# Kernel optimization log

Hardware: AMD Instinct MI355X
Metric: run time of the kernel (lower is better)

The kernel has to match this reference:

```python
import jax, jax.numpy as jnp
import numpy as np

B, D_MODEL, FEAT = 2, 96, 128
SSM_RATIO, D_STATE, NDIR, CGROUP = 2.0, 16, 4, 12
D_INNER = int(SSM_RATIO * D_MODEL)  # 192


def _conv1x1(x, w):
    # x: (B, Cin, H, W), w: (Cout, Cin)
    return jnp.einsum('bchw,oc->bohw', x, w)


def _normalize_w(Gl, Gm, Gr):
    gl, gm, gr = jax.nn.sigmoid(Gl), jax.nn.sigmoid(Gm), jax.nn.sigmoid(Gr)
    s = gl + gm + gr
    # top row has no (i-1) neighbor, bottom row has no (i+1) neighbor
    s = s.at[:, :, 0, :].set(gm[:, :, 0, :] + gr[:, :, 0, :])
    s = s.at[:, :, -1, :].set(gl[:, :, -1, :] + gm[:, :, -1, :])
    s = jnp.maximum(s, 1e-7)
    return gl / s, gm / s, gr / s


def _spn_scan(X, l, Gl, Gm, Gr):
    # Gated tridiagonal 2D recurrence, left-to-right over W:
    # h[i,t] = l[i,t]*x[i,t] + Gl[i,t]*h[i-1,t-1] + Gm[i,t]*h[i,t-1] + Gr[i,t]*h[i+1,t-1]
    seq = tuple(jnp.moveaxis(a, -1, 0) for a in (X, l, Gl, Gm, Gr))  # (W, B, C, H)
    h0 = jnp.zeros(X.shape[:-1], X.dtype)  # (B, C, H)

    def step(h, t):
        x_t, l_t, gl_t, gm_t, gr_t = t
        zero = jnp.zeros_like(h[..., :1])
        h_up = jnp.concatenate([zero, h[..., :-1]], axis=-1)  # h[i-1]
        h_dn = jnp.concatenate([h[..., 1:], zero], axis=-1)   # h[i+1]
        h = l_t * x_t + gl_t * h_up + gm_t * h + gr_t * h_dn
        return h, h

    _, ys = jax.lax.scan(step, h0, seq)
    return jnp.moveaxis(ys, 0, -1)  # (B, C, H, W)


def setup_inputs() -> dict:
    key = jax.random.key(0)
    ks = jax.random.split(key, 16)

    def w(k, shape):
        fan_in = int(np.prod(shape[1:])) if len(shape) > 1 else shape[0]
        return jax.random.normal(k, shape, jnp.float32) * (fan_in ** -0.5)

    return {
        'x': jax.random.normal(ks[0], (B, D_MODEL, FEAT, FEAT), jnp.float32),
        'w_in': w(ks[1], (D_INNER, D_MODEL)),
        'w_dw': w(ks[2], (D_INNER, 1, 3, 3)),
        'b_dw': jnp.zeros((D_INNER,), jnp.float32),
        'w_xdown': w(ks[3], (D_STATE, D_INNER)),
        'w_wup': w(ks[4], (CGROUP * D_INNER, D_STATE)),
        'w_lup': w(ks[5], (NDIR * D_INNER, D_STATE)),
        'w_uup': w(ks[6], (NDIR * D_INNER, D_STATE)),
        'w_ddown': w(ks[7], (NDIR * D_INNER, D_STATE)),
        'w_m': w(ks[8], (NDIR,)),
        'grn_gamma': jnp.zeros((1, D_INNER, 1, 1), jnp.float32),
        'grn_beta': jnp.zeros((1, D_INNER, 1, 1), jnp.float32),
        'ln_w': jnp.ones((D_INNER,), jnp.float32),
        'ln_b': jnp.zeros((D_INNER,), jnp.float32),
        'w_out': w(ks[9], (D_MODEL, D_INNER)),
    }


def reference(x, w_in, w_dw, b_dw, w_xdown, w_wup, w_lup, w_uup, w_ddown, w_m,
              grn_gamma, grn_beta, ln_w, ln_b, w_out):
    Bq, _, H, W = x.shape
    # in_proj (Linear2d) then depthwise 3x3 conv (note: self.act is unused in forward)
    x1 = _conv1x1(x, w_in)
    x1 = jax.lax.conv_general_dilated(
        x1, w_dw, (1, 1), 'SAME', feature_group_count=D_INNER,
        dimension_numbers=('NCHW', 'OIHW', 'NCHW')) + b_dw[None, :, None, None]
    # low-rank gate/lambda/gain/skip projections through d_state bottleneck
    xp = _conv1x1(x1, w_xdown)          # (B, 16, H, W)
    ws = _conv1x1(xp, w_wup)            # (B, 12*D_INNER, H, W)
    Ls = _conv1x1(xp, w_lup)
    Us = _conv1x1(xp, w_uup)
    Ds = _conv1x1(xp, w_ddown)
    # 4 directional views stacked on channels (direction-major layout)
    xt = jnp.swapaxes(x1, 2, 3)  # requires H == W
    xs = jnp.concatenate([x1, xt, x1[..., ::-1], xt[..., ::-1]], axis=1)  # (B, 4*D_INNER, H, W)
    DC = NDIR * D_INNER
    gl, gm, gr = _normalize_w(ws[:, :DC], ws[:, DC:2 * DC], ws[:, 2 * DC:])
    out = _spn_scan(xs, Ls, gl, gm, gr)
    out = out * Us + xs * Ds
    # merge directions with 1x1 conv over the 4 direction channels
    y = jnp.einsum('bnchw,n->bchw', out.reshape(Bq, NDIR, D_INNER, H, W), w_m)
    # LayerNorm2d over channels (eps 1e-5)
    mu = y.mean(axis=1, keepdims=True)
    var = y.var(axis=1, keepdims=True)
    y = (y - mu) / jnp.sqrt(var + 1e-5) * ln_w[None, :, None, None] + ln_b[None, :, None, None]
    # GRN
    Gx = jnp.sqrt(jnp.sum(y * y, axis=(2, 3), keepdims=True))
    Nx = Gx / (Gx.mean(axis=1, keepdims=True) + 1e-6)
    y = grn_gamma * (y * Nx) + grn_beta + y
    return _conv1x1(y, w_out)
```

## Files before the change

kernel.cpp:

```cpp
#include <hip/hip_runtime.h>

typedef float v2f __attribute__((ext_vector_type(2)));

constexpr int BB = 2;
constexpr int CM = 96;
constexpr int CI = 192;
constexpr int NPIX = 128 * 128;
constexpr int DS = 16;
constexpr int DC = 4 * CI;

constexpr size_t OFF_X1PRE = 0;
constexpr size_t OFF_X1    = 6291456;
constexpr size_t OFF_X1T   = 12582912;
constexpr size_t OFF_XP    = 18874368;
constexpr size_t OFF_YPA   = 19398656;
constexpr size_t OFF_YPB   = 0;
constexpr size_t OFF_YM    = 12582912;
constexpr size_t OFF_MU    = 18874368;
constexpr size_t OFF_RSTD  = 18874368 + 32768;
constexpr size_t OFF_YT    = 6291456;
constexpr size_t OFF_GXS   = 25690112;

__device__ __forceinline__ float frcp(float x) { return __builtin_amdgcn_rcpf(x); }
__device__ __forceinline__ float sigm(float x) { return frcp(1.f + __expf(-x)); }

__global__ __launch_bounds__(256) void k1_conv_in(const float* __restrict__ x,
                                                  const float* __restrict__ w_in,
                                                  float* __restrict__ x1pre) {
    __shared__ float xs[16][128];
    __shared__ float wsh[16][32];
    int pt = blockIdx.x;
    int b = pt >> 7;
    int pxb = (pt & 127) * 128;
    int cb = blockIdx.y * 32;
    int tid = threadIdx.x;
    int cl0 = (tid >> 5) * 4;
    int px0 = (tid & 31) * 4;
    float acc[4][4];
#pragma unroll
    for (int i = 0; i < 4; i++)
#pragma unroll
        for (int j = 0; j < 4; j++) acc[i][j] = 0.f;

    for (int m0 = 0; m0 < 96; m0 += 16) {
        {
            int e = tid * 8;
            int ml = e >> 7, pp = e & 127;
            const float* src = &x[((size_t)(b * CM + m0 + ml)) * NPIX + pxb + pp];
            float4 v0 = *(const float4*)(src);
            float4 v1 = *(const float4*)(src + 4);
            *(float4*)&xs[ml][pp] = v0;
            *(float4*)&xs[ml][pp + 4] = v1;
        }
        if (tid < 128) {
            int cl = tid >> 2, mq = (tid & 3) * 4;
            float4 v = *(const float4*)&w_in[(size_t)(cb + cl) * CM + m0 + mq];
            wsh[mq + 0][cl] = v.x; wsh[mq + 1][cl] = v.y;
            wsh[mq + 2][cl] = v.z; wsh[mq + 3][cl] = v.w;
        }
        __syncthreads();
#pragma unroll
        for (int m = 0; m < 16; m++) {
            float4 wv = *(const float4*)&wsh[m][cl0];
            float4 xv = *(const float4*)&xs[m][px0];
            float wr[4] = {wv.x, wv.y, wv.z, wv.w};
            float xr[4] = {xv.x, xv.y, xv.z, xv.w};
#pragma unroll
            for (int i = 0; i < 4; i++)
#pragma unroll
                for (int j = 0; j < 4; j++) acc[i][j] += wr[i] * xr[j];
        }
        __syncthreads();
    }
#pragma unroll
    for (int i = 0; i < 4; i++) {
        float4 v = {acc[i][0], acc[i][1], acc[i][2], acc[i][3]};
        *(float4*)&x1pre[((size_t)(b * CI + cb + cl0 + i)) * NPIX + pxb + px0] = v;
    }
}

__global__ __launch_bounds__(256) void k2_dwconv(const float* __restrict__ x1pre,
                                                 const float* __restrict__ w_dw,
                                                 const float* __restrict__ b_dw,
                                                 float* __restrict__ x1,
                                                 float* __restrict__ x1T) {
    __shared__ float inT[66][67];
    __shared__ float outT[64][65];
    int blk = blockIdx.x;
    int bc = blk >> 2;
    int tile = blk & 3;
    int h0 = (tile >> 1) * 64, w0 = (tile & 1) * 64;
    int c = bc % CI;
    const float* src = x1pre + (size_t)bc * NPIX;
    int tid = threadIdx.x;
    for (int idx = tid; idx < 66 * 66; idx += 256) {
        int r = idx / 66, cl = idx - r * 66;
        int hh = h0 - 1 + r, ww = w0 - 1 + cl;
        float v = 0.f;
        if ((unsigned)hh < 128u && (unsigned)ww < 128u) v = src[hh * 128 + ww];
        inT[r][cl] = v;
    }
    float w00 = w_dw[c * 9 + 0], w01 = w_dw[c * 9 + 1], w02 = w_dw[c * 9 + 2];
    float w10 = w_dw[c * 9 + 3], w11 = w_dw[c * 9 + 4], w12 = w_dw[c * 9 + 5];
    float w20 = w_dw[c * 9 + 6], w21 = w_dw[c * 9 + 7], w22 = w_dw[c * 9 + 8];
    float bias = b_dw[c];
    __syncthreads();
    int cl = tid & 63, r0 = tid >> 6;
#pragma unroll 4
    for (int k = 0; k < 16; k++) {
        int r = k * 4 + r0;
        float s = w00 * inT[r][cl]     + w01 * inT[r][cl + 1]     + w02 * inT[r][cl + 2]
                + w10 * inT[r + 1][cl] + w11 * inT[r + 1][cl + 1] + w12 * inT[r + 1][cl + 2]
                + w20 * inT[r + 2][cl] + w21 * inT[r + 2][cl + 1] + w22 * inT[r + 2][cl + 2]
                + bias;
        x1[(size_t)bc * NPIX + (h0 + r) * 128 + w0 + cl] = s;
        outT[r][cl] = s;
    }
    __syncthreads();
#pragma unroll 4
    for (int k = 0; k < 16; k++) {
        int r = k * 4 + r0;
        x1T[(size_t)bc * NPIX + (w0 + r) * 128 + h0 + cl] = outT[cl][r];
    }
}

__global__ __launch_bounds__(256) void k3_xp(const float* __restrict__ x1T,
                                             const float* __restrict__ w_xdown,
                                             float* __restrict__ xp) {
    __shared__ float wsh[DS * CI];
    __shared__ float ph[DS][128];
    int blk = blockIdx.x;
    int b = blk >> 7, t = blk & 127;
    int tid = threadIdx.x;
    for (int e = tid * 4; e < DS * CI; e += 1024) {
        *(float4*)&wsh[e] = *(const float4*)&w_xdown[e];
    }
    __syncthreads();
    int i = tid & 127;
    int half = tid >> 7;
    int c0 = half * 96;
    float acc[DS];
#pragma unroll
    for (int s = 0; s < DS; s++) acc[s] = 0.f;
    const float* xbase = x1T + ((size_t)b * CI + c0) * NPIX + t * 128 + i;
#pragma unroll 4
    for (int c = 0; c < 96; c++) {
        float v = xbase[(size_t)c * NPIX];
#pragma unroll
        for (int s = 0; s < DS; s++) acc[s] += wsh[s * CI + c0 + c] * v;
    }
    if (half == 1) {
#pragma unroll
        for (int s = 0; s < DS; s++) ph[s][i] = acc[s];
    }
    __syncthreads();
    if (half == 0) {
        float out[DS];
#pragma unroll
        for (int s = 0; s < DS; s++) out[s] = acc[s] + ph[s][i];
        float4* dst = (float4*)&xp[(((size_t)b * 128 + t) * 128 + i) * DS];
#pragma unroll
        for (int q = 0; q < 4; q++) dst[q] = *(float4*)&out[q * 4];
    }
}

__global__ __launch_bounds__(256, 3) void k4_scan(
        const float* __restrict__ x1, const float* __restrict__ x1T,
        const float* __restrict__ xp,
        const float* __restrict__ w_wup, const float* __restrict__ w_lup,
        const float* __restrict__ w_uup, const float* __restrict__ w_ddown,
        const float* __restrict__ w_m,
        float* __restrict__ ypA, float* __restrict__ ypB) {
    __shared__ float ycol[2][2][128];
    __shared__ float seam[2][2][2];
    int blk = blockIdx.x;
    int parity = blk & 1;
    int bc = blk >> 1;
    int c = bc % CI;
    int b = bc / CI;
    int tid = threadIdx.x;
    int dl = tid >> 7;
    int half = (tid >> 6) & 1;
    int l = tid & 63;
    int i = half * 64 + l;
    int dir = __builtin_amdgcn_readfirstlane(parity + 2 * dl);
    const float* xsrc = (parity ? x1 : x1T) + (size_t)bc * NPIX;
    float* yp = (parity ? ypB : ypA) + (size_t)bc * NPIX;

    int q = dir * CI + c;
    float wm = w_m[dir];
    v2f wGl[8], wGm[8], wGr[8], wL[8], wU[8], wD[8];
#pragma unroll
    for (int j = 0; j < 8; j++) {
        float2 a;
        a = *(const float2*)&w_wup[(size_t)q * DS + 2 * j];            wGl[j] = v2f{a.x, a.y};
        a = *(const float2*)&w_wup[(size_t)(DC + q) * DS + 2 * j];     wGm[j] = v2f{a.x, a.y};
        a = *(const float2*)&w_wup[(size_t)(2 * DC + q) * DS + 2 * j]; wGr[j] = v2f{a.x, a.y};
        a = *(const float2*)&w_lup[(size_t)q * DS + 2 * j];            wL[j]  = v2f{a.x, a.y};
        a = *(const float2*)&w_uup[(size_t)q * DS + 2 * j];            wU[j]  = v2f{a.x * wm, a.y * wm};
        a = *(const float2*)&w_ddown[(size_t)q * DS + 2 * j];          wD[j]  = v2f{a.x * wm, a.y * wm};
    }
    if (tid < 8) ((float*)seam)[tid] = 0.f;
    __syncthreads();

    const float* xpb = xp + ((size_t)b * 128 * 128 + i) * DS;
    auto xaddr = [&](int t) {
        int tt = dl ? (127 - t) : t;
        return xsrc + tt * 128 + i;
    };

    float4 g0, g1, g2, g3;
    {
        const float4* p = (const float4*)xpb;
        g0 = p[0]; g1 = p[1]; g2 = p[2]; g3 = p[3];
    }
    float Xc = *xaddr(0);
    float Xn = *xaddr(1);

    float h = 0.f;
    for (int t = 0; t < 128; t++) {
        int buf = t & 1;
        float4 n0, n1, n2, n3;
        float Xn2 = 0.f;
        if (t < 127) {
            const float4* p = (const float4*)(xpb + (size_t)(t + 1) * 2048);
            n0 = p[0]; n1 = p[1]; n2 = p[2]; n3 = p[3];
        }
        if (t < 126) Xn2 = *xaddr(t + 2);

        v2f xv[8] = {v2f{g0.x, g0.y}, v2f{g0.z, g0.w}, v2f{g1.x, g1.y}, v2f{g1.z, g1.w},
                     v2f{g2.x, g2.y}, v2f{g2.z, g2.w}, v2f{g3.x, g3.y}, v2f{g3.z, g3.w}};
        v2f aGl = v2f{0.f, 0.f}, aGm = aGl, aGr = aGl, aL = aGl, aU = aGl, aD = aGl;
#pragma unroll
        for (int j = 0; j < 8; j++) {
            v2f xa = xv[j];
            aGl += wGl[j] * xa; aGm += wGm[j] * xa; aGr += wGr[j] * xa;
            aL  += wL[j] * xa;  aU  += wU[j] * xa;  aD  += wD[j] * xa;
        }
        float sGl = aGl.x + aGl.y, sGm = aGm.x + aGm.y, sGr = aGr.x + aGr.y;
        float sL = aL.x + aL.y, sU = aU.x + aU.y, sD = aD.x + aD.y;
        float gl = sigm(sGl), gm = sigm(sGm), gr = sigm(sGr);
        float ss = (i == 0) ? (gm + gr) : (i == 127) ? (gl + gm) : (gl + gm + gr);
        float inv = frcp(fmaxf(ss, 1e-7f));
        float up = __shfl_up(h, 1);
        if (l == 0) up = half ? seam[buf ^ 1][dl][0] : 0.f;
        float dn = __shfl_down(h, 1);
        if (l == 63) dn = half ? 0.f : seam[buf ^ 1][dl][1];
        float X = Xc;
        h = sL * X + inv * (gl * up + gm * h + gr * dn);
        ycol[buf][dl][i] = h * sU + X * sD;
        if (half == 0 && l == 63) seam[buf][dl][0] = h;
        if (half == 1 && l == 0)  seam[buf][dl][1] = h;
        __syncthreads();
        if (tid < 128) {
            yp[t * 128 + tid] = ycol[buf][0][tid] + ycol[buf][1][tid];
        }
        g0 = n0; g1 = n1; g2 = n2; g3 = n3;
        Xc = Xn; Xn = Xn2;
    }
}

__global__ __launch_bounds__(256) void k5a_stats(const float* __restrict__ ypA,
                                                 const float* __restrict__ ypB,
                                                 float* __restrict__ ym,
                                                 float* __restrict__ mu,
                                                 float* __restrict__ rstd) {
    __shared__ float s_sum[4][64];
    __shared__ float s_ssq[4][64];
    int blk = blockIdx.x;
    int b = blk >> 8;
    int px0 = (blk & 255) * 64;
    int tid = threadIdx.x;
    int pl = tid & 63, cp = tid >> 6;
    int c0 = cp * 48;
    size_t base = ((size_t)b * CI + c0) * NPIX + px0 + pl;
    const float* pa = ypA + base;
    const float* pb = ypB + base;
    float* pm = ym + base;
    float sum = 0.f, ssq = 0.f;
#pragma unroll 8
    for (int j = 0; j < 48; j++) {
        float v = pa[(size_t)j * NPIX] + pb[(size_t)j * NPIX];
        pm[(size_t)j * NPIX] = v;
        sum += v; ssq += v * v;
    }
    s_sum[cp][pl] = sum; s_ssq[cp][pl] = ssq;
    __syncthreads();
    if (tid < 64) {
        float s = s_sum[0][tid] + s_sum[1][tid] + s_sum[2][tid] + s_sum[3][tid];
        float q = s_ssq[0][tid] + s_ssq[1][tid] + s_ssq[2][tid] + s_ssq[3][tid];
        float m = s * (1.f / 192.f);
        float var = q * (1.f / 192.f) - m * m;
        mu[(size_t)b * NPIX + px0 + tid] = m;
        rstd[(size_t)b * NPIX + px0 + tid] = rsqrtf(var + 1e-5f);
    }
}

__global__ __launch_bounds__(256) void k5b_norm(const float* __restrict__ ym,
                                                const float* __restrict__ mu,
                                                const float* __restrict__ rstd,
                                                const float* __restrict__ ln_w,
                                                const float* __restrict__ ln_b,
                                                float* __restrict__ yt,
                                                float* __restrict__ gxs) {
    __shared__ float red[4];
    int blk = blockIdx.x;
    int ph = blk & 1;
    int bc = blk >> 1;
    int c = bc % CI;
    int b = bc / CI;
    const float* ymp = ym + (size_t)bc * NPIX;
    const float* mup = mu + (size_t)b * NPIX;
    const float* rsp = rstd + (size_t)b * NPIX;
    float* ytp = yt + (size_t)bc * NPIX;
    int tid = threadIdx.x;
    float lw = ln_w[c], lb = ln_b[c];
    float acc = 0.f;
#pragma unroll
    for (int it = 0; it < 8; it++) {
        int p = ph * 8192 + it * 1024 + tid * 4;
        float4 v = *(const float4*)&ymp[p];
        float4 m = *(const float4*)&mup[p];
        float4 r = *(const float4*)&rsp[p];
        float4 vn;
        vn.x = (v.x - m.x) * r.x * lw + lb;
        vn.y = (v.y - m.y) * r.y * lw + lb;
        vn.z = (v.z - m.z) * r.z * lw + lb;
        vn.w = (v.w - m.w) * r.w * lw + lb;
        *(float4*)&ytp[p] = vn;
        acc += vn.x * vn.x + vn.y * vn.y + vn.z * vn.z + vn.w * vn.w;
    }
#pragma unroll
    for (int m = 1; m < 64; m <<= 1) acc += __shfl_xor(acc, m);
    if ((tid & 63) == 0) red[tid >> 6] = acc;
    __syncthreads();
    if (tid == 0) {
        atomicAdd(&gxs[bc], red[0] + red[1] + red[2] + red[3]);
    }
}

__global__ __launch_bounds__(256) void k6_out(
        const float* __restrict__ yt, const float* __restrict__ gxs,
        const float* __restrict__ grn_gamma, const float* __restrict__ grn_beta,
        const float* __restrict__ w_out, float* __restrict__ outp) {
    __shared__ float scale_s[CI];
    __shared__ float beta_s[CI];
    __shared__ float redv[1];
    __shared__ float stage[96 * 16 * 8];
    int blk = blockIdx.x;
    int b = blk >> 7;
    int rest = blk & 127;
    int i0 = (rest >> 4) * 16;
    int t0 = (rest & 15) * 8;
    int tid = threadIdx.x;
    if (tid < CI) scale_s[tid] = sqrtf(gxs[b * CI + tid]);
    __syncthreads();
    if (tid < 64) {
        float p = scale_s[tid] + scale_s[tid + 64] + scale_s[tid + 128];
#pragma unroll
        for (int m = 1; m < 64; m <<= 1) p += __shfl_xor(p, m);
        if (tid == 0) redv[0] = p * (1.f / 192.f);
    }
    __syncthreads();
    float mean = redv[0];
    if (tid < CI) {
        float nx = scale_s[tid] / (mean + 1e-6f);
        scale_s[tid] = 1.f + grn_gamma[tid] * nx;
        beta_s[tid] = grn_beta[tid];
    }
    __syncthreads();

    int og = tid >> 6;
    int o0 = og * 24;
    int pg = tid & 63;
    int tt = pg >> 3;
    int ii0 = (pg & 7) * 2;
    float acc[24][2];
#pragma unroll
    for (int j = 0; j < 24; j++) { acc[j][0] = 0.f; acc[j][1] = 0.f; }
    const float* ybase = yt + ((size_t)b * CI) * NPIX + (t0 + tt) * 128 + (i0 + ii0);
#pragma unroll 2
    for (int cc = 0; cc < CI; cc++) {
        float2 yv = *(const float2*)&ybase[(size_t)cc * NPIX];
        float sc = scale_s[cc], be = beta_s[cc];
        float y0 = yv.x * sc + be, y1 = yv.y * sc + be;
#pragma unroll
        for (int j = 0; j < 24; j++) {
            float wv = w_out[(size_t)(o0 + j) * CI + cc];
            acc[j][0] += wv * y0; acc[j][1] += wv * y1;
        }
    }
#pragma unroll
    for (int j = 0; j < 24; j++) {
        stage[((o0 + j) * 16 + ii0 + 0) * 8 + tt] = acc[j][0];
        stage[((o0 + j) * 16 + ii0 + 1) * 8 + tt] = acc[j][1];
    }
    __syncthreads();
    for (int k = 0; k < 48; k++) {
        int L = k * 256 + tid;
        int o = L >> 7;
        int r = L & 127;
        int ii = r >> 3, t2 = r & 7;
        outp[((size_t)(b * CM + o)) * NPIX + (i0 + ii) * 128 + (t0 + t2)] = stage[L];
    }
}

extern "C" void kernel_launch(void* const* d_in, const int* in_sizes, int n_in,
                              void* d_out, int out_size, void* d_ws, size_t ws_size,
                              hipStream_t stream) {
    const float* x        = (const float*)d_in[0];
    const float* w_in     = (const float*)d_in[1];
    const float* w_dw     = (const float*)d_in[2];
    const float* b_dw     = (const float*)d_in[3];
    const float* w_xdown  = (const float*)d_in[4];
    const float* w_wup    = (const float*)d_in[5];
    const float* w_lup    = (const float*)d_in[6];
    const float* w_uup    = (const float*)d_in[7];
    const float* w_ddown  = (const float*)d_in[8];
    const float* w_m      = (const float*)d_in[9];
    const float* grn_gamma= (const float*)d_in[10];
    const float* grn_beta = (const float*)d_in[11];
    const float* ln_w     = (const float*)d_in[12];
    const float* ln_b     = (const float*)d_in[13];
    const float* w_out    = (const float*)d_in[14];
    float* ws    = (float*)d_ws;
    float* x1pre = ws + OFF_X1PRE;
    float* x1    = ws + OFF_X1;
    float* x1T   = ws + OFF_X1T;
    float* xp    = ws + OFF_XP;
    float* ypA   = ws + OFF_YPA;
    float* ypB   = ws + OFF_YPB;
    float* ym    = ws + OFF_YM;
    float* mu    = ws + OFF_MU;
    float* rstd  = ws + OFF_RSTD;
    float* yt    = ws + OFF_YT;
    float* gxs   = ws + OFF_GXS;
    float* outp  = (float*)d_out;

    hipMemsetAsync(gxs, 0, BB * CI * sizeof(float), stream);
    dim3 g1(256, 6);
    k1_conv_in<<<g1, 256, 0, stream>>>(x, w_in, x1pre);
    k2_dwconv<<<BB * CI * 4, 256, 0, stream>>>(x1pre, w_dw, b_dw, x1, x1T);
    k3_xp<<<BB * 128, 256, 0, stream>>>(x1T, w_xdown, xp);
    k4_scan<<<BB * CI * 2, 256, 0, stream>>>(x1, x1T, xp, w_wup, w_lup, w_uup,
                                             w_ddown, w_m, ypA, ypB);
    k5a_stats<<<BB * 256, 256, 0, stream>>>(ypA, ypB, ym, mu, rstd);
    k5b_norm<<<BB * CI * 2, 256, 0, stream>>>(ym, mu, rstd, ln_w, ln_b, yt, gxs);
    k6_out<<<256, 256, 0, stream>>>(yt, gxs, grn_gamma, grn_beta, w_out, outp);
}
```

Baseline: 297.6 us.

## Split xp and stats kernels finer, unroll scan by two with algebraic gate normalization

k3_xp now launches four times as many blocks, each handling 32 pixels across 8 channel groups. The weights are transposed in shared memory for float4 reads, and the partial sums are reduced through shared memory. k4_scan is unrolled by two timesteps with double-buffered register prefetch of xp and x. It replaces the three sigmoids plus the normalization with a single reciprocal of products of (1+exp) terms. k5a_stats uses 2x more blocks and issues all loads up front. The goal is more parallelism in the small kernels and shorter per-step latency in the serial scan, at the cost of more register pressure and a clamp on the exp argument that slightly changes numerics.

```diff
diff --git a/kernel.cpp b/kernel.cpp
--- a/kernel.cpp
+++ b/kernel.cpp
@@ -22,7 +22,6 @@
 constexpr size_t OFF_GXS   = 25690112;
 
 __device__ __forceinline__ float frcp(float x) { return __builtin_amdgcn_rcpf(x); }
-__device__ __forceinline__ float sigm(float x) { return frcp(1.f + __expf(-x)); }
 
 __global__ __launch_bounds__(256) void k1_conv_in(const float* __restrict__ x,
                                                   const float* __restrict__ w_in,
@@ -127,42 +126,63 @@
 __global__ __launch_bounds__(256) void k3_xp(const float* __restrict__ x1T,
                                              const float* __restrict__ w_xdown,
                                              float* __restrict__ xp) {
-    __shared__ float wsh[DS * CI];
-    __shared__ float ph[DS][128];
+    __shared__ float wsh_t[CI * DS];
+    __shared__ float red[8][32][20];
     int blk = blockIdx.x;
-    int b = blk >> 7, t = blk & 127;
-    int tid = threadIdx.x;
-    for (int e = tid * 4; e < DS * CI; e += 1024) {
-        *(float4*)&wsh[e] = *(const float4*)&w_xdown[e];
-    }
-    __syncthreads();
-    int i = tid & 127;
-    int half = tid >> 7;
-    int c0 = half * 96;
+    int b = blk >> 9;
+    int rest = blk & 511;
+    int t = rest >> 2;
+    int hq = rest & 3;
+    int tid = threadIdx.x;
+#pragma unroll
+    for (int rep = 0; rep < 12; rep++) {
+        int e = rep * 256 + tid;
+        int s = e / CI;
+        int cc = e - s * CI;
+        wsh_t[cc * DS + s] = w_xdown[e];
+    }
+    int pl = tid & 31;
+    int cg = tid >> 5;
+    int c0 = cg * 24;
+    int hpix = hq * 32 + pl;
+    __syncthreads();
     float acc[DS];
 #pragma unroll
     for (int s = 0; s < DS; s++) acc[s] = 0.f;
-    const float* xbase = x1T + ((size_t)b * CI + c0) * NPIX + t * 128 + i;
+    const float* xb = x1T + ((size_t)b * CI + c0) * NPIX + t * 128 + hpix;
 #pragma unroll 4
-    for (int c = 0; c < 96; c++) {
-        float v = xbase[(size_t)c * NPIX];
-#pragma unroll
-        for (int s = 0; s < DS; s++) acc[s] += wsh[s * CI + c0 + c] * v;
-    }
-    if (half == 1) {
-#pragma unroll
-        for (int s = 0; s < DS; s++) ph[s][i] = acc[s];
-    }
-    __syncthreads();
-    if (half == 0) {
-        float out[DS];
-#pragma unroll
-        for (int s = 0; s < DS; s++) out[s] = acc[s] + ph[s][i];
-        float4* dst = (float4*)&xp[(((size_t)b * 128 + t) * 128 + i) * DS];
-#pragma unroll
-        for (int q = 0; q < 4; q++) dst[q] = *(float4*)&out[q * 4];
-    }
-}
+    for (int cc = 0; cc < 24; cc++) {
+        float v = xb[(size_t)cc * NPIX];
+        const float4* wr4 = (const float4*)&wsh_t[(c0 + cc) * DS];
+        float4 w0 = wr4[0], w1 = wr4[1], w2 = wr4[2], w3 = wr4[3];
+        acc[0] = fmaf(w0.x, v, acc[0]);  acc[1] = fmaf(w0.y, v, acc[1]);
+        acc[2] = fmaf(w0.z, v, acc[2]);  acc[3] = fmaf(w0.w, v, acc[3]);
+        acc[4] = fmaf(w1.x, v, acc[4]);  acc[5] = fmaf(w1.y, v, acc[5]);
+        acc[6] = fmaf(w1.z, v, acc[6]);  acc[7] = fmaf(w1.w, v, acc[7]);
+        acc[8] = fmaf(w2.x, v, acc[8]);  acc[9] = fmaf(w2.y, v, acc[9]);
+        acc[10] = fmaf(w2.z, v, acc[10]); acc[11] = fmaf(w2.w, v, acc[11]);
+        acc[12] = fmaf(w3.x, v, acc[12]); acc[13] = fmaf(w3.y, v, acc[13]);
+        acc[14] = fmaf(w3.z, v, acc[14]); acc[15] = fmaf(w3.w, v, acc[15]);
+    }
+#pragma unroll
+    for (int q = 0; q < 4; q++)
+        *(float4*)&red[cg][pl][q * 4] = *(float4*)&acc[q * 4];
+    __syncthreads();
+    int px = tid >> 3;
+    int s2 = (tid & 7) * 2;
+    float r0 = 0.f, r1 = 0.f;
+#pragma unroll
+    for (int g = 0; g < 8; g++) { r0 += red[g][px][s2]; r1 += red[g][px][s2 + 1]; }
+    float2 o2 = {r0, r1};
+    *(float2*)&xp[(((size_t)b * 128 + t) * 128 + hq * 32 + px) * DS + s2] = o2;
+}
+
+#define GLOAD(P, ptr) { const v2f* _gp = (const v2f*)(ptr);                  \
+    P##0 = _gp[0]; P##1 = _gp[1]; P##2 = _gp[2]; P##3 = _gp[3];              \
+    P##4 = _gp[4]; P##5 = _gp[5]; P##6 = _gp[6]; P##7 = _gp[7]; }
+
+#define DACC(j, P) { aGl += wGl[j] * P; aGm += wGm[j] * P; aGr += wGr[j] * P; \
+    aL += wL[j] * P; aU += wU[j] * P; aD += wD[j] * P; }
 
 __global__ __launch_bounds__(256, 3) void k4_scan(
         const float* __restrict__ x1, const float* __restrict__ x1T,
@@ -203,60 +223,89 @@
     if (tid < 8) ((float*)seam)[tid] = 0.f;
     __syncthreads();
 
-    const float* xpb = xp + ((size_t)b * 128 * 128 + i) * DS;
-    auto xaddr = [&](int t) {
-        int tt = dl ? (127 - t) : t;
-        return xsrc + tt * 128 + i;
-    };
-
-    float4 g0, g1, g2, g3;
-    {
-        const float4* p = (const float4*)xpb;
-        g0 = p[0]; g1 = p[1]; g2 = p[2]; g3 = p[3];
-    }
-    float Xc = *xaddr(0);
-    float Xn = *xaddr(1);
+    bool at_top = (i == 0), at_bot = (i == 127);
+    bool seam_lo = (half == 0 && l == 63);
+    bool seam_hi = (half == 1 && l == 0);
+
+    const float* gbase = xp + ((size_t)b * NPIX + i) * DS;
+    const float* gptr = gbase + 4096;
+    int xstep = dl ? -128 : 128;
+    int xstep2 = 2 * xstep;
+    const float* xpe = xsrc + (dl ? 127 * 128 : 0) + i;
+    const float* xpo = xpe + xstep;
+    float* ypp = yp + (tid & 127);
+
+    v2f e0, e1, e2, e3, e4, e5, e6, e7;
+    v2f o0, o1, o2, o3, o4, o5, o6, o7;
+    GLOAD(e, gbase);
+    GLOAD(o, gbase + 2048);
+    float Xe = xpe[0];
+    float Xo = xpo[0];
 
     float h = 0.f;
-    for (int t = 0; t < 128; t++) {
-        int buf = t & 1;
-        float4 n0, n1, n2, n3;
-        float Xn2 = 0.f;
-        if (t < 127) {
-            const float4* p = (const float4*)(xpb + (size_t)(t + 1) * 2048);
-            n0 = p[0]; n1 = p[1]; n2 = p[2]; n3 = p[3];
+    for (int t = 0; t < 128; t += 2) {
+        {
+            v2f aGl = wGl[0] * e0, aGm = wGm[0] * e0, aGr = wGr[0] * e0;
+            v2f aL = wL[0] * e0, aU = wU[0] * e0, aD = wD[0] * e0;
+            DACC(1, e1) DACC(2, e2) DACC(3, e3) DACC(4, e4)
+            DACC(5, e5) DACC(6, e6) DACC(7, e7)
+            GLOAD(e, gptr);
+            float sGl = aGl.x + aGl.y, sGm = aGm.x + aGm.y, sGr = aGr.x + aGr.y;
+            float sL = aL.x + aL.y, sU = aU.x + aU.y, sD = aD.x + aD.y;
+            float el = __expf(fminf(-sGl, 40.f));
+            float em = __expf(fminf(-sGm, 40.f));
+            float er = __expf(fminf(-sGr, 40.f));
+            float tl = 1.f + el, tm = 1.f + em, tr = 1.f + er;
+            float nl = at_top ? 0.f : tm * tr;
+            float nm = tl * tr;
+            float nr = at_bot ? 0.f : tl * tm;
+            float inv = frcp(nl + nm + nr);
+            float up = __shfl_up(h, 1);
+            if (l == 0) up = half ? seam[1][dl][0] : 0.f;
+            float dn = __shfl_down(h, 1);
+            if (l == 63) dn = half ? 0.f : seam[1][dl][1];
+            float X = Xe;
+            h = fmaf(sL, X, (nl * up + nm * h + nr * dn) * inv);
+            Xe = xpe[xstep2];
+            ycol[0][dl][i] = fmaf(h, sU, X * sD);
+            if (seam_lo) seam[0][dl][0] = h;
+            if (seam_hi) seam[0][dl][1] = h;
         }
-        if (t < 126) Xn2 = *xaddr(t + 2);
-
-        v2f xv[8] = {v2f{g0.x, g0.y}, v2f{g0.z, g0.w}, v2f{g1.x, g1.y}, v2f{g1.z, g1.w},
-                     v2f{g2.x, g2.y}, v2f{g2.z, g2.w}, v2f{g3.x, g3.y}, v2f{g3.z, g3.w}};
-        v2f aGl = v2f{0.f, 0.f}, aGm = aGl, aGr = aGl, aL = aGl, aU = aGl, aD = aGl;
-#pragma unroll
-        for (int j = 0; j < 8; j++) {
-            v2f xa = xv[j];
-            aGl += wGl[j] * xa; aGm += wGm[j] * xa; aGr += wGr[j] * xa;
-            aL  += wL[j] * xa;  aU  += wU[j] * xa;  aD  += wD[j] * xa;
+        __syncthreads();
+        if (tid < 128) ypp[0] = ycol[0][0][tid] + ycol[0][1][tid];
+        {
+            v2f aGl = wGl[0] * o0, aGm = wGm[0] * o0, aGr = wGr[0] * o0;
+            v2f aL = wL[0] * o0, aU = wU[0] * o0, aD = wD[0] * o0;
+            DACC(1, o1) DACC(2, o2) DACC(3, o3) DACC(4, o4)
+            DACC(5, o5) DACC(6, o6) DACC(7, o7)
+            GLOAD(o, gptr + 2048);
+            float sGl = aGl.x + aGl.y, sGm = aGm.x + aGm.y, sGr = aGr.x + aGr.y;
+            float sL = aL.x + aL.y, sU = aU.x + aU.y, sD = aD.x + aD.y;
+            float el = __expf(fminf(-sGl, 40.f));
+            float em = __expf(fminf(-sGm, 40.f));
+            float er = __expf(fminf(-sGr, 40.f));
+            float tl = 1.f + el, tm = 1.f + em, tr = 1.f + er;
+            float nl = at_top ? 0.f : tm * tr;
+            float nm = tl * tr;
+            float nr = at_bot ? 0.f : tl * tm;
+            float inv = frcp(nl + nm + nr);
+            float up = __shfl_up(h, 1);
+            if (l == 0) up = half ? seam[0][dl][0] : 0.f;
+            float dn = __shfl_down(h, 1);
+            if (l == 63) dn = half ? 0.f : seam[0][dl][1];
+            float X = Xo;
+            h = fmaf(sL, X, (nl * up + nm * h + nr * dn) * inv);
+            Xo = xpo[xstep2];
+            ycol[1][dl][i] = fmaf(h, sU, X * sD);
+            if (seam_lo) seam[1][dl][0] = h;
+            if (seam_hi) seam[1][dl][1] = h;
         }
-        float sGl = aGl.x + aGl.y, sGm = aGm.x + aGm.y, sGr = aGr.x + aGr.y;
-        float sL = aL.x + aL.y, sU = aU.x + aU.y, sD = aD.x + aD.y;
-        float gl = sigm(sGl), gm = sigm(sGm), gr = sigm(sGr);
-        float ss = (i == 0) ? (gm + gr) : (i == 127) ? (gl + gm) : (gl + gm + gr);
-        float inv = frcp(fmaxf(ss, 1e-7f));
-        float up = __shfl_up(h, 1);
-        if (l == 0) up = half ? seam[buf ^ 1][dl][0] : 0.f;
-        float dn = __shfl_down(h, 1);
-        if (l == 63) dn = half ? 0.f : seam[buf ^ 1][dl][1];
-        float X = Xc;
-        h = sL * X + inv * (gl * up + gm * h + gr * dn);
-        ycol[buf][dl][i] = h * sU + X * sD;
-        if (half == 0 && l == 63) seam[buf][dl][0] = h;
-        if (half == 1 && l == 0)  seam[buf][dl][1] = h;
+        gptr += 4096;
+        xpe += xstep2;
+        xpo += xstep2;
         __syncthreads();
-        if (tid < 128) {
-            yp[t * 128 + tid] = ycol[buf][0][tid] + ycol[buf][1][tid];
-        }
-        g0 = n0; g1 = n1; g2 = n2; g3 = n3;
-        Xc = Xn; Xn = Xn2;
+        if (tid < 128) ypp[128] = ycol[1][0][tid] + ycol[1][1][tid];
+        ypp += 256;
     }
 }
 
@@ -265,32 +314,39 @@
                                                  float* __restrict__ ym,
                                                  float* __restrict__ mu,
                                                  float* __restrict__ rstd) {
-    __shared__ float s_sum[4][64];
-    __shared__ float s_ssq[4][64];
+    __shared__ float s_sum[8][32];
+    __shared__ float s_ssq[8][32];
     int blk = blockIdx.x;
-    int b = blk >> 8;
-    int px0 = (blk & 255) * 64;
-    int tid = threadIdx.x;
-    int pl = tid & 63, cp = tid >> 6;
-    int c0 = cp * 48;
+    int b = blk >> 9;
+    int px0 = (blk & 511) * 32;
+    int tid = threadIdx.x;
+    int pl = tid & 31, cg = tid >> 5;
+    int c0 = cg * 24;
     size_t base = ((size_t)b * CI + c0) * NPIX + px0 + pl;
     const float* pa = ypA + base;
     const float* pb = ypB + base;
     float* pm = ym + base;
+    float va[24], vb[24];
+#pragma unroll
+    for (int j = 0; j < 24; j++) va[j] = pa[(size_t)j * NPIX];
+#pragma unroll
+    for (int j = 0; j < 24; j++) vb[j] = pb[(size_t)j * NPIX];
     float sum = 0.f, ssq = 0.f;
-#pragma unroll 8
-    for (int j = 0; j < 48; j++) {
-        float v = pa[(size_t)j * NPIX] + pb[(size_t)j * NPIX];
+#pragma unroll
+    for (int j = 0; j < 24; j++) {
+        float v = va[j] + vb[j];
         pm[(size_t)j * NPIX] = v;
-        sum += v; ssq += v * v;
-    }
-    s_sum[cp][pl] = sum; s_ssq[cp][pl] = ssq;
-    __syncthreads();
-    if (tid < 64) {
-        float s = s_sum[0][tid] + s_sum[1][tid] + s_sum[2][tid] + s_sum[3][tid];
-        float q = s_ssq[0][tid] + s_ssq[1][tid] + s_ssq[2][tid] + s_ssq[3][tid];
+        sum += v;
+        ssq = fmaf(v, v, ssq);
+    }
+    s_sum[cg][pl] = sum; s_ssq[cg][pl] = ssq;
+    __syncthreads();
+    if (tid < 32) {
+        float s = 0.f, qq = 0.f;
+#pragma unroll
+        for (int g = 0; g < 8; g++) { s += s_sum[g][tid]; qq += s_ssq[g][tid]; }
         float m = s * (1.f / 192.f);
-        float var = q * (1.f / 192.f) - m * m;
+        float var = qq * (1.f / 192.f) - m * m;
         mu[(size_t)b * NPIX + px0 + tid] = m;
         rstd[(size_t)b * NPIX + px0 + tid] = rsqrtf(var + 1e-5f);
     }
@@ -441,10 +497,10 @@
     dim3 g1(256, 6);
     k1_conv_in<<<g1, 256, 0, stream>>>(x, w_in, x1pre);
     k2_dwconv<<<BB * CI * 4, 256, 0, stream>>>(x1pre, w_dw, b_dw, x1, x1T);
-    k3_xp<<<BB * 128, 256, 0, stream>>>(x1T, w_xdown, xp);
+    k3_xp<<<BB * 128 * 4, 256, 0, stream>>>(x1T, w_xdown, xp);
     k4_scan<<<BB * CI * 2, 256, 0, stream>>>(x1, x1T, xp, w_wup, w_lup, w_uup,
                                              w_ddown, w_m, ypA, ypB);
-    k5a_stats<<<BB * 256, 256, 0, stream>>>(ypA, ypB, ym, mu, rstd);
+    k5a_stats<<<BB * 512, 256, 0, stream>>>(ypA, ypB, ym, mu, rstd);
     k5b_norm<<<BB * CI * 2, 256, 0, stream>>>(ym, mu, rstd, ln_w, ln_b, yt, gxs);
     k6_out<<<256, 256, 0, stream>>>(yt, gxs, grn_gamma, grn_beta, w_out, outp);
 }
```

Result: faster. 277.2 us (-6.8%).
